# Optimization experiments

Hardware: AMD Instinct MI355X
Metric: run time of the kernel (lower is better)

The kernel has to match this reference:

```python
import jax, jax.numpy as jnp
import numpy as np

# ---- constants from the source module ----
NB = [[0,1,2,3],[0,1,4],[0,2,5],[0,3,6],[1,4,7],[2,5,8],[3,6,9],[4,7,10],[5,8,11],[6,9],[7,10],[8,11],[12,13,14,15],[12,13,16],[12,14,17],[12,15],[13,16,18],[14,17,19],[16,18,20],[17,19,21],[18,20,22],[19,21,23],[20,22],[21,23]]
PARENT = np.array([0,0,0,0,1,2,3,4,5,6,7,8,9,9,9,12,13,14,16,17,18,19,20,21])  # root parent sentinel handled separately
KJ, NV, PREG = 24, 6890, 200
LEN = np.array([len(n) for n in NB])
NBR_IDX = np.zeros((KJ,4), np.int32)
NBR_VALID = np.zeros((KJ,4), np.float32)
for k, n in enumerate(NB):
    NBR_IDX[k,:len(n)] = n; NBR_VALID[k,:len(n)] = 1.0
BETA_POS = np.zeros((KJ,17), np.float32); BETA_POS[np.arange(KJ), 4*LEN] = 1.0
SLICE_MASK = np.zeros((23,17), np.float32)
for j in range(23):
    SLICE_MASK[j,:4*LEN[j]+1] = 1.0  # self.K[j] has 4*len(NB[j])+1 rows
NBR_IDX = jnp.asarray(NBR_IDX); NBR_VALID = jnp.asarray(NBR_VALID)
BETA_POS = jnp.asarray(BETA_POS); SLICE_MASK = jnpp = jnp.asarray(SLICE_MASK)


def setup_inputs() -> dict:
    key = jax.random.key(0)
    ks = jax.random.split(key, 9)
    V = jax.random.normal(ks[0], (PREG, NV, 3), jnp.float32)
    T = jax.random.normal(ks[1], (PREG, NV, 3), jnp.float32)
    J = jax.random.normal(ks[2], (PREG, KJ, 3), jnp.float32)
    theta = 0.3 * jax.random.normal(ks[3], (PREG, 72), jnp.float32)
    W_prime = jax.random.uniform(ks[4], (NV, KJ), jnp.float32)
    W_i = jax.random.uniform(ks[5], (NV, KJ), jnp.float32)
    W_i = W_i / W_i.sum(axis=1, keepdims=True)
    A = jax.random.uniform(ks[6], (23, NV), jnp.float32)
    K_mats = 0.01 * jax.random.normal(ks[7], (23, 17, 3 * NV), jnp.float32)
    K_mats = K_mats * SLICE_MASK[:, :, None]  # zero rows beyond the ragged per-joint size
    beta_2 = jnp.ones((1,), jnp.float32)
    return {"V": V, "T": T, "J": J, "theta": theta, "W_prime": W_prime, "W_i": W_i, "A": A, "K_mats": K_mats, "beta_2": beta_2, "epoch": 1}


def _rodrigues(pose):  # pose: (K,3)
    angle = jnp.maximum(jnp.linalg.norm(pose, axis=1, keepdims=True), 1e-8)
    axis = pose / angle
    x, y, z = axis[:, 0], axis[:, 1], axis[:, 2]
    zero = jnp.zeros_like(x)
    skew = jnp.stack([zero, -z, y, z, zero, -x, -y, x, zero], axis=1).reshape(-1, 3, 3)
    outer = axis[:, :, None] * axis[:, None, :]
    c = jnp.cos(angle)[:, :, None]
    s = jnp.sin(angle)[:, :, None]
    eye = jnp.eye(3, dtype=pose.dtype)[None]
    return c * eye + (1.0 - c) * outer + s * skew


def _compute_G(pose72, Jp):  # pose72: (72,), Jp: (K,3) -> (K,4,4)
    R = _rodrigues(pose72.reshape(KJ, 3))
    t = Jp - jnp.concatenate([jnp.zeros((1, 3), Jp.dtype), Jp[PARENT[1:]]], axis=0)
    G_local = jnp.zeros((KJ, 4, 4), Jp.dtype)
    G_local = G_local.at[:, :3, :3].set(R).at[:, :3, 3].set(t).at[:, 3, 3].set(1.0)
    Gs = [G_local[0]]
    for i in range(1, KJ):  # fixed 24-joint kinematic tree
        Gs.append(Gs[PARENT[i]] @ G_local[i])
    G = jnp.stack(Gs, axis=0)
    off = jnp.einsum('kij,kj->ki', G[:, :3, :3], Jp)  # homogeneous w=0 -> rotation only
    return G.at[:, :3, 3].add(-off)


def _axis2quat(p):  # (M,3) -> (M,4)
    angle = jnp.sqrt(jnp.maximum(jnp.sum(p ** 2, axis=1), 1e-16))
    n = p / angle[:, None]
    s = jnp.sin(angle / 2)
    return jnp.stack([n[:, 0] * s, n[:, 1] * s, n[:, 2] * s, jnp.cos(angle / 2) - 1.0], axis=1)


def reference(V, T, J, theta, W_prime, W_i, A, K_mats, beta_2, epoch):
    P = V.shape[0]
    b2 = beta_2[0]
    # normalized skinning weights
    W_relu = jax.nn.relu(W_prime)
    W_change = W_relu / (W_relu.sum(axis=1, keepdims=True) + 1e-8)
    # per-pose global joint transforms
    G_prime = jax.vmap(_compute_G)(theta, J)  # (P,K,4,4)
    # quaternion features and blend-shape correction
    q = _axis2quat(theta.reshape(P * KJ, 3)).reshape(P, KJ, 4)
    qg = q[:, NBR_IDX, :] * NBR_VALID[None, :, :, None]       # (P,K,4,4) neighbor gather
    q17 = jnp.concatenate([qg.reshape(P, KJ, 16), jnp.zeros((P, KJ, 1), q.dtype)], axis=-1)
    q17 = q17 + BETA_POS[None] * b2                            # beta_2 at column 4*len
    qm = q17[:, 1:, :] * SLICE_MASK[None]                      # ragged slice q_ne[:, j+1, :lenK]
    contrib = jnp.einsum('pjl,jlm->pjm', qm, K_mats).reshape(P, 23, NV, 3)
    T_p = jnp.einsum('pjnc,jn->pnc', contrib, jax.nn.relu(A)) + T
    # linear blend skinning
    T_h = jnp.concatenate([T_p, jnp.ones((P, NV, 1), T_p.dtype)], axis=-1)
    transformed = jnp.einsum('pkij,pnj->pnki', G_prime[:, :, :3, :], T_h)  # (P,N,K,3)
    verts = jnp.einsum('nk,pnkc->pnc', W_change, transformed)
    # energies
    e = float(epoch)
    g_wi = 0.1 * np.exp(-0.1 * e)
    g_w = 0.002 * np.exp(-0.008 * e)
    g_a = 0.001 * np.exp(-0.008 * e)
    g_k = 0.1 * np.exp(-0.008 * e)
    E_D = jnp.sum((V - verts) ** 2)
    E_Wi = jnp.sum((W_change - W_i) ** 2)
    E_W = jnp.sum(jnp.abs(W_change))
    E_A = jnp.sum(jnp.abs(A))
    E_K = jnp.sum(jnp.sqrt(jnp.sum(K_mats ** 2, axis=(1, 2))))
    E = E_D + g_wi * E_Wi + g_w * E_W + g_a * E_A + g_k * E_K
    return (E, verts)
```

## Files before the change

kernel.cpp:

```cpp
#include <hip/hip_runtime.h>
#include <math.h>

#define KJ 24
#define NV 6890
#define PREG 200
#define M_TOT (NV*3)
#define KDIM 391
#define KPAD 416
#define TP_STRIDE 20672
#define NMTILE 323

#define EDP_OFF 0
#define EKP_OFF 2816
#define WIP_OFF 10248
#define EWP_OFF 10280
#define EAP_OFF 10312
#define RED_OFF 10344
#define G_OFF   10384
#define WT_OFF  67984
#define RA_OFF  233344
#define QBH_OFF_U 1417600
#define QBL_OFF_U 1524096
#define TP_OFF  815296

typedef __attribute__((ext_vector_type(8))) short short8;
typedef __attribute__((ext_vector_type(4))) float f32x4;

__constant__ int c_PARENT[24] = {0,0,0,0,1,2,3,4,5,6,7,8,9,9,9,12,13,14,16,17,18,19,20,21};
__constant__ int c_DEPTH[24]  = {0,1,1,1,2,2,2,3,3,3,4,4,4,4,4,5,5,5,6,6,7,7,8,8};
__constant__ int c_LEN[24]    = {4,3,3,3,3,3,3,3,3,2,2,2,4,3,3,2,3,3,3,3,3,3,2,2};
__constant__ int c_NBR[24][4] = {
  {0,1,2,3},{0,1,4,0},{0,2,5,0},{0,3,6,0},{1,4,7,0},{2,5,8,0},{3,6,9,0},{4,7,10,0},
  {5,8,11,0},{6,9,0,0},{7,10,0,0},{8,11,0,0},{12,13,14,15},{12,13,16,0},{12,14,17,0},
  {12,15,0,0},{13,16,18,0},{14,17,19,0},{16,18,20,0},{17,19,21,0},{18,20,22,0},
  {19,21,23,0},{20,22,0,0},{21,23,0,0}};

__device__ __forceinline__ float waveReduce(float v) {
  #pragma unroll
  for (int off = 32; off > 0; off >>= 1) v += __shfl_down(v, off, 64);
  return v;
}
__device__ __forceinline__ unsigned short f2bf(float x) {
  union { float f; unsigned u; } v; v.f = x;
  unsigned r = v.u + 0x7FFFu + ((v.u >> 16) & 1u);
  return (unsigned short)(r >> 16);
}
__device__ __forceinline__ float bf2f(unsigned short h) {
  union { unsigned u; float f; } v; v.u = ((unsigned)h) << 16; return v.f;
}

__global__ __launch_bounds__(256) void kPre(const float* __restrict__ J,
                                            const float* __restrict__ theta,
                                            const float* __restrict__ beta2,
                                            const float* __restrict__ Wp,
                                            const float* __restrict__ Wi,
                                            const float* __restrict__ A,
                                            float* __restrict__ ws) {
  unsigned short* qbh = (unsigned short*)ws + QBH_OFF_U;
  unsigned short* qbl = (unsigned short*)ws + QBL_OFF_U;
  int b = blockIdx.x;
  if (b < 50) {
    __shared__ float Gl[4][24][12];
    __shared__ float Gg[4][24][12];
    __shared__ float q[4][24][4];
    int w = threadIdx.x >> 6, t = threadIdx.x & 63;
    int p = b*4 + w;
    if (t < 24) {
      float x = theta[p*72 + 3*t + 0];
      float y = theta[p*72 + 3*t + 1];
      float z = theta[p*72 + 3*t + 2];
      float n2 = x*x + y*y + z*z;
      float ang = fmaxf(sqrtf(n2), 1e-8f);
      float ia = 1.f/ang;
      float ax = x*ia, ay = y*ia, az = z*ia;
      float c = cosf(ang), s = sinf(ang), C = 1.f - c;
      float jx = J[p*72+3*t], jy = J[p*72+3*t+1], jz = J[p*72+3*t+2];
      float tx = jx, ty = jy, tz = jz;
      if (t > 0) {
        int par = c_PARENT[t];
        tx -= J[p*72+3*par]; ty -= J[p*72+3*par+1]; tz -= J[p*72+3*par+2];
      }
      Gl[w][t][0]=c+C*ax*ax;   Gl[w][t][1]=C*ax*ay-s*az; Gl[w][t][2]=C*ax*az+s*ay; Gl[w][t][3]=tx;
      Gl[w][t][4]=C*ax*ay+s*az;Gl[w][t][5]=c+C*ay*ay;    Gl[w][t][6]=C*ay*az-s*ax; Gl[w][t][7]=ty;
      Gl[w][t][8]=C*ax*az-s*ay;Gl[w][t][9]=C*ay*az+s*ax; Gl[w][t][10]=c+C*az*az;   Gl[w][t][11]=tz;
      float ang2 = sqrtf(fmaxf(n2, 1e-16f));
      float inv2 = 1.f/ang2;
      float s2 = sinf(0.5f*ang2);
      q[w][t][0] = x*inv2*s2; q[w][t][1] = y*inv2*s2; q[w][t][2] = z*inv2*s2;
      q[w][t][3] = cosf(0.5f*ang2) - 1.f;
    }
    __syncthreads();
    for (int lev = 0; lev <= 8; lev++) {
      if (t < 24 && c_DEPTH[t] == lev) {
        if (lev == 0) {
          for (int i2 = 0; i2 < 12; i2++) Gg[w][0][i2] = Gl[w][0][i2];
        } else {
          int par = c_PARENT[t];
          for (int r = 0; r < 3; r++) {
            float g0 = Gg[w][par][r*4+0], g1 = Gg[w][par][r*4+1];
            float g2 = Gg[w][par][r*4+2], g3 = Gg[w][par][r*4+3];
            for (int c2 = 0; c2 < 4; c2++) {
              float v = g0*Gl[w][t][0+c2] + g1*Gl[w][t][4+c2] + g2*Gl[w][t][8+c2];
              if (c2 == 3) v += g3;
              Gg[w][t][r*4+c2] = v;
            }
          }
        }
      }
      __syncthreads();
    }
    if (t < 24) {
      float jx = J[p*72+3*t], jy = J[p*72+3*t+1], jz = J[p*72+3*t+2];
      float* gp = ws + G_OFF + p*288 + t*12;
      #pragma unroll
      for (int r = 0; r < 3; r++) {
        float off = Gg[w][t][r*4+0]*jx + Gg[w][t][r*4+1]*jy + Gg[w][t][r*4+2]*jz;
        Gg[w][t][r*4+3] -= off;
      }
      #pragma unroll
      for (int i2 = 0; i2 < 12; i2++) gp[i2] = Gg[w][t][i2];
    }
    __syncthreads();
    float b2 = beta2[0];
    for (int e = t; e < KDIM; e += 64) {
      int j = e / 17, l = e - 17*j;
      int k = j + 1;
      float val = 0.f;
      if (l < 4*c_LEN[j] + 1) {
        if (l < 16) {
          int sidx = l >> 2, cc = l & 3;
          if (sidx < c_LEN[k]) val = q[w][c_NBR[k][sidx]][cc];
        }
        if (l == 4*c_LEN[k]) val += b2;
      }
      unsigned short hi = f2bf(val);
      unsigned short lo = f2bf(val - bf2f(hi));
      qbh[p*KPAD + e] = hi;
      qbl[p*KPAD + e] = lo;
    }
    for (int e = KDIM + t; e < KPAD; e += 64) {
      qbh[p*KPAD + e] = 0; qbl[p*KPAD + e] = 0;
    }
  } else {
    int d = b - 50;
    int t = threadIdx.x;
    int n = d*256 + t;
    float ewi = 0.f, ew = 0.f, ea = 0.f;
    if (n < NV) {
      float wv[24]; float sum = 0.f;
      const float4* wp4 = (const float4*)(Wp + n*24);
      #pragma unroll
      for (int i = 0; i < 6; i++) {
        float4 v4 = wp4[i];
        wv[4*i+0] = fmaxf(v4.x, 0.f); wv[4*i+1] = fmaxf(v4.y, 0.f);
        wv[4*i+2] = fmaxf(v4.z, 0.f); wv[4*i+3] = fmaxf(v4.w, 0.f);
        sum += wv[4*i+0]+wv[4*i+1]+wv[4*i+2]+wv[4*i+3];
      }
      float inv = 1.f/(sum + 1e-8f);
      #pragma unroll
      for (int k = 0; k < 24; k++) {
        float wc = wv[k]*inv;
        ws[WT_OFF + k*NV + n] = wc;
        ew += fabsf(wc);
        float dd = wc - Wi[n*24+k];
        ewi += dd*dd;
      }
    }
    for (int i = d*256 + t; i < 23*NV; i += 27*256) ea += fabsf(A[i]);
    for (int i = d*256 + t; i < 23*TP_STRIDE; i += 27*256) {
      int j = i / TP_STRIDE, m = i - j*TP_STRIDE;
      float v = 0.f;
      if (m < M_TOT) v = fmaxf(A[j*NV + m/3], 0.f);
      ws[RA_OFF + i] = v;
    }
    for (int i = d*256 + t; i < 56*KPAD; i += 27*256) {
      qbh[200*KPAD + i] = 0; qbl[200*KPAD + i] = 0;
    }
    __shared__ float red[3][4];
    int lane = t & 63, wv2 = t >> 6;
    ewi = waveReduce(ewi); ew = waveReduce(ew); ea = waveReduce(ea);
    if (lane == 0) { red[0][wv2] = ewi; red[1][wv2] = ew; red[2][wv2] = ea; }
    __syncthreads();
    if (t == 0) {
      ws[WIP_OFF + d] = red[0][0]+red[0][1]+red[0][2]+red[0][3];
      ws[EWP_OFF + d] = red[1][0]+red[1][1]+red[1][2]+red[1][3];
      ws[EAP_OFF + d] = red[2][0]+red[2][1]+red[2][2]+red[2][3];
    }
  }
}

__global__ __launch_bounds__(256) void kB(const float* __restrict__ K,
                                          float* __restrict__ ws) {
  __shared__ unsigned short Bh[64*32];
  __shared__ unsigned short Bl[64*32];
  __shared__ float ek[23];
  const unsigned short* qbh = (const unsigned short*)ws + QBH_OFF_U;
  const unsigned short* qbl = (const unsigned short*)ws + QBL_OFF_U;
  float* __restrict__ TP = ws + TP_OFF;

  const int tid = threadIdx.x;
  const int bx = blockIdx.x;
  const int py = blockIdx.y;
  const int m0 = bx * 64;
  const int w = tid >> 6, lane = tid & 63;
  const int r = lane & 15, qd = lane >> 4;
  const int pbase = py*128 + w*32;
  const int c4 = tid & 15, pr = tid >> 4;

  if (tid < 23) ek[tid] = 0.f;
  __syncthreads();

  f32x4 acc[2][4];
  #pragma unroll
  for (int h = 0; h < 2; h++)
    #pragma unroll
    for (int f = 0; f < 4; f++) acc[h][f] = (f32x4){0.f,0.f,0.f,0.f};

  const int aoff0 = (pbase + r) * KPAD + qd * 8;
  const int aoff1 = aoff0 + 16 * KPAD;

  for (int ks = 0; ks < 13; ks++) {
    if (ks) __syncthreads();
    {
      int mm = m0 + 4*c4;
      int kg0 = ks*32 + 2*pr, kg1 = kg0 + 1;
      float ka[4] = {0,0,0,0}, kb[4] = {0,0,0,0};
      float wa[4] = {0,0,0,0}, wb[4] = {0,0,0,0};
      float sq0 = 0.f, sq1 = 0.f;
      if (kg0 < KDIM) {
        int j = kg0 / 17;
        const float* kr = K + (size_t)kg0*M_TOT + mm;
        if (mm + 3 < M_TOT) {
          float2 x = *(const float2*)kr; float2 y = *(const float2*)(kr+2);
          ka[0]=x.x; ka[1]=x.y; ka[2]=y.x; ka[3]=y.y;
        } else {
          #pragma unroll
          for (int i = 0; i < 4; i++) if (mm+i < M_TOT) ka[i] = kr[i];
        }
        const float* rr = ws + RA_OFF + (size_t)j*TP_STRIDE + mm;
        float4 ra = *(const float4*)rr;
        wa[0]=ka[0]*ra.x; wa[1]=ka[1]*ra.y; wa[2]=ka[2]*ra.z; wa[3]=ka[3]*ra.w;
        sq0 = ka[0]*ka[0]+ka[1]*ka[1]+ka[2]*ka[2]+ka[3]*ka[3];
      }
      if (kg1 < KDIM) {
        int j = kg1 / 17;
        const float* kr = K + (size_t)kg1*M_TOT + mm;
        if (mm + 3 < M_TOT) {
          float2 x = *(const float2*)kr; float2 y = *(const float2*)(kr+2);
          kb[0]=x.x; kb[1]=x.y; kb[2]=y.x; kb[3]=y.y;
        } else {
          #pragma unroll
          for (int i = 0; i < 4; i++) if (mm+i < M_TOT) kb[i] = kr[i];
        }
        const float* rr = ws + RA_OFF + (size_t)j*TP_STRIDE + mm;
        float4 ra = *(const float4*)rr;
        wb[0]=kb[0]*ra.x; wb[1]=kb[1]*ra.y; wb[2]=kb[2]*ra.z; wb[3]=kb[3]*ra.w;
        sq1 = kb[0]*kb[0]+kb[1]*kb[1]+kb[2]*kb[2]+kb[3]*kb[3];
      }
      #pragma unroll
      for (int i = 0; i < 4; i++) {
        unsigned short h0 = f2bf(wa[i]); unsigned short l0 = f2bf(wa[i] - bf2f(h0));
        unsigned short h1 = f2bf(wb[i]); unsigned short l1 = f2bf(wb[i] - bf2f(h1));
        int mi = 4*c4 + i;
        int physdw = (pr + 4*(c4 & 3)) & 15;
        *(unsigned*)&Bh[mi*32 + physdw*2] = (unsigned)h0 | ((unsigned)h1 << 16);
        *(unsigned*)&Bl[mi*32 + physdw*2] = (unsigned)l0 | ((unsigned)l1 << 16);
      }
      if (py == 0) {
        #pragma unroll
        for (int off = 1; off <= 8; off <<= 1) {
          sq0 += __shfl_xor(sq0, off, 64);
          sq1 += __shfl_xor(sq1, off, 64);
        }
        if ((lane & 15) == 0) {
          if (kg0 < KDIM) atomicAdd(&ek[kg0/17], sq0);
          if (kg1 < KDIM) atomicAdd(&ek[kg1/17], sq1);
        }
      }
    }
    __syncthreads();
    {
      int kso = ks * 32;
      short8 ah0 = *(const short8*)(qbh + aoff0 + kso);
      short8 ah1 = *(const short8*)(qbh + aoff1 + kso);
      short8 al0 = *(const short8*)(qbl + aoff0 + kso);
      short8 al1 = *(const short8*)(qbl + aoff1 + kso);
      short8 bh[4], bl[4];
      const int rotdw = 4*((r >> 2) & 3);
      #pragma unroll
      for (int f = 0; f < 4; f++) {
        int m = f*16 + r;
        int physdw = (4*qd + rotdw) & 15;
        bh[f] = *(const short8*)(&Bh[m*32 + physdw*2]);
        bl[f] = *(const short8*)(&Bl[m*32 + physdw*2]);
      }
      #pragma unroll
      for (int f = 0; f < 4; f++) {
        acc[0][f] = __builtin_amdgcn_mfma_f32_16x16x32_bf16(ah0, bh[f], acc[0][f], 0, 0, 0);
        acc[1][f] = __builtin_amdgcn_mfma_f32_16x16x32_bf16(ah1, bh[f], acc[1][f], 0, 0, 0);
      }
      #pragma unroll
      for (int f = 0; f < 4; f++) {
        acc[0][f] = __builtin_amdgcn_mfma_f32_16x16x32_bf16(ah0, bl[f], acc[0][f], 0, 0, 0);
        acc[1][f] = __builtin_amdgcn_mfma_f32_16x16x32_bf16(ah1, bl[f], acc[1][f], 0, 0, 0);
      }
      #pragma unroll
      for (int f = 0; f < 4; f++) {
        acc[0][f] = __builtin_amdgcn_mfma_f32_16x16x32_bf16(al0, bh[f], acc[0][f], 0, 0, 0);
        acc[1][f] = __builtin_amdgcn_mfma_f32_16x16x32_bf16(al1, bh[f], acc[1][f], 0, 0, 0);
      }
    }
  }
  #pragma unroll
  for (int h = 0; h < 2; h++)
    #pragma unroll
    for (int f = 0; f < 4; f++)
      #pragma unroll
      for (int g = 0; g < 4; g++) {
        int p = pbase + h*16 + qd*4 + g;
        TP[(size_t)p*TP_STRIDE + m0 + f*16 + r] = acc[h][f][g];
      }
  __syncthreads();
  if (py == 0 && tid < 23)
    ws[EKP_OFF + tid*NMTILE + bx] = ek[tid];
}

__global__ __launch_bounds__(256) void kC(const float* __restrict__ V,
                                          const float* __restrict__ T,
                                          float* __restrict__ ws,
                                          float* __restrict__ out) {
  int p = blockIdx.y;
  int n0 = (blockIdx.x*256 + threadIdx.x) * 2;
  __shared__ float Gs[288];
  __shared__ float tmp[4];
  if (threadIdx.x < 72)
    ((float4*)Gs)[threadIdx.x] = ((const float4*)(ws + G_OFF + p*288))[threadIdx.x];
  __syncthreads();
  float ed = 0.f;
  if (n0 < NV) {
    float M0[12], M1[12];
    #pragma unroll
    for (int i = 0; i < 12; i++) { M0[i] = 0.f; M1[i] = 0.f; }
    const float* Wt = ws + WT_OFF;
    #pragma unroll
    for (int k = 0; k < 24; k++) {
      float2 wv = *(const float2*)(Wt + k*NV + n0);
      float4 g0 = *(const float4*)(Gs + k*12 + 0);
      float4 g1 = *(const float4*)(Gs + k*12 + 4);
      float4 g2 = *(const float4*)(Gs + k*12 + 8);
      M0[0] = fmaf(wv.x, g0.x, M0[0]); M0[1]  = fmaf(wv.x, g0.y, M0[1]);
      M0[2] = fmaf(wv.x, g0.z, M0[2]); M0[3]  = fmaf(wv.x, g0.w, M0[3]);
      M0[4] = fmaf(wv.x, g1.x, M0[4]); M0[5]  = fmaf(wv.x, g1.y, M0[5]);
      M0[6] = fmaf(wv.x, g1.z, M0[6]); M0[7]  = fmaf(wv.x, g1.w, M0[7]);
      M0[8] = fmaf(wv.x, g2.x, M0[8]); M0[9]  = fmaf(wv.x, g2.y, M0[9]);
      M0[10]= fmaf(wv.x, g2.z, M0[10]);M0[11] = fmaf(wv.x, g2.w, M0[11]);
      M1[0] = fmaf(wv.y, g0.x, M1[0]); M1[1]  = fmaf(wv.y, g0.y, M1[1]);
      M1[2] = fmaf(wv.y, g0.z, M1[2]); M1[3]  = fmaf(wv.y, g0.w, M1[3]);
      M1[4] = fmaf(wv.y, g1.x, M1[4]); M1[5]  = fmaf(wv.y, g1.y, M1[5]);
      M1[6] = fmaf(wv.y, g1.z, M1[6]); M1[7]  = fmaf(wv.y, g1.w, M1[7]);
      M1[8] = fmaf(wv.y, g2.x, M1[8]); M1[9]  = fmaf(wv.y, g2.y, M1[9]);
      M1[10]= fmaf(wv.y, g2.z, M1[10]);M1[11] = fmaf(wv.y, g2.w, M1[11]);
    }
    size_t tb = (size_t)p*M_TOT + 3*n0;
    size_t pb = (size_t)p*TP_STRIDE + 3*n0;
    float2 q0 = *(const float2*)(ws + TP_OFF + pb);
    float2 q1 = *(const float2*)(ws + TP_OFF + pb + 2);
    float2 q2 = *(const float2*)(ws + TP_OFF + pb + 4);
    float2 s0 = *(const float2*)(T + tb);
    float2 s1 = *(const float2*)(T + tb + 2);
    float2 s2 = *(const float2*)(T + tb + 4);
    float ta0 = q0.x + s0.x, ta1 = q0.y + s0.y, ta2 = q1.x + s1.x;
    float tb0 = q1.y + s1.y, tb1 = q2.x + s2.x, tb2 = q2.y + s2.y;
    float v00 = M0[0]*ta0 + M0[1]*ta1 + M0[2]*ta2  + M0[3];
    float v01 = M0[4]*ta0 + M0[5]*ta1 + M0[6]*ta2  + M0[7];
    float v02 = M0[8]*ta0 + M0[9]*ta1 + M0[10]*ta2 + M0[11];
    float v10 = M1[0]*tb0 + M1[1]*tb1 + M1[2]*tb2  + M1[3];
    float v11 = M1[4]*tb0 + M1[5]*tb1 + M1[6]*tb2  + M1[7];
    float v12 = M1[8]*tb0 + M1[9]*tb1 + M1[10]*tb2 + M1[11];
    out[1+tb+0] = v00; out[1+tb+1] = v01; out[1+tb+2] = v02;
    out[1+tb+3] = v10; out[1+tb+4] = v11; out[1+tb+5] = v12;
    float2 x0 = *(const float2*)(V + tb);
    float2 x1 = *(const float2*)(V + tb + 2);
    float2 x2 = *(const float2*)(V + tb + 4);
    float d0 = x0.x-v00, d1 = x0.y-v01, d2 = x1.x-v02;
    float d3 = x1.y-v10, d4 = x2.x-v11, d5 = x2.y-v12;
    ed = d0*d0 + d1*d1 + d2*d2 + d3*d3 + d4*d4 + d5*d5;
  }
  ed = waveReduce(ed);
  int lane = threadIdx.x & 63, w = threadIdx.x >> 6;
  if (lane == 0) tmp[w] = ed;
  __syncthreads();
  if (threadIdx.x == 0)
    ws[EDP_OFF + blockIdx.y*14 + blockIdx.x] = tmp[0]+tmp[1]+tmp[2]+tmp[3];
}

__global__ __launch_bounds__(256) void kF1(float* __restrict__ ws) {
  __shared__ float sb[4];
  int b = blockIdx.x, t = threadIdx.x, lane = t & 63, w = t >> 6;
  if (b < 23) {
    float s = 0.f;
    for (int i = t; i < NMTILE; i += 256) s += ws[EKP_OFF + b*NMTILE + i];
    s = waveReduce(s);
    if (lane == 0) sb[w] = s;
    __syncthreads();
    if (t == 0) ws[RED_OFF + b] = sb[0]+sb[1]+sb[2]+sb[3];
  } else if (b == 23) {
    float s = 0.f;
    for (int i = t; i < 2800; i += 256) s += ws[EDP_OFF + i];
    s = waveReduce(s);
    if (lane == 0) sb[w] = s;
    __syncthreads();
    if (t == 0) ws[RED_OFF + 23] = sb[0]+sb[1]+sb[2]+sb[3];
  } else {
    if (w == 0) {
      float s = (lane < 27) ? ws[WIP_OFF + lane] : 0.f;
      s = waveReduce(s);
      if (lane == 0) ws[RED_OFF + 24] = s;
    } else if (w == 1) {
      float s = (lane < 27) ? ws[EWP_OFF + lane] : 0.f;
      s = waveReduce(s);
      if (lane == 0) ws[RED_OFF + 25] = s;
    } else if (w == 2) {
      float s = (lane < 27) ? ws[EAP_OFF + lane] : 0.f;
      s = waveReduce(s);
      if (lane == 0) ws[RED_OFF + 26] = s;
    }
  }
}

__global__ void kF2(const int* __restrict__ epoch, const float* __restrict__ ws,
                    float* __restrict__ out) {
  int t = threadIdx.x;
  float s = (t < 23) ? sqrtf(ws[RED_OFF + t]) : 0.f;
  s = waveReduce(s);
  if (t == 0) {
    float e    = (float)epoch[0];
    float g_wi = 0.1f   * expf(-0.1f  * e);
    float g_w  = 0.002f * expf(-0.008f* e);
    float g_a  = 0.001f * expf(-0.008f* e);
    float g_k  = 0.1f   * expf(-0.008f* e);
    out[0] = ws[RED_OFF+23] + g_wi*ws[RED_OFF+24] + g_w*ws[RED_OFF+25]
           + g_a*ws[RED_OFF+26] + g_k*s;
  }
}

extern "C" void kernel_launch(void* const* d_in, const int* in_sizes, int n_in,
                              void* d_out, int out_size, void* d_ws, size_t ws_size,
                              hipStream_t stream) {
  const float* V     = (const float*)d_in[0];
  const float* T     = (const float*)d_in[1];
  const float* J     = (const float*)d_in[2];
  const float* theta = (const float*)d_in[3];
  const float* Wp    = (const float*)d_in[4];
  const float* Wi    = (const float*)d_in[5];
  const float* A     = (const float*)d_in[6];
  const float* K     = (const float*)d_in[7];
  const float* b2    = (const float*)d_in[8];
  const int*   epoch = (const int*)d_in[9];
  float* out = (float*)d_out;
  float* ws  = (float*)d_ws;

  hipLaunchKernelGGL(kPre, dim3(77),         dim3(256), 0, stream,
                     J, theta, b2, Wp, Wi, A, ws);
  hipLaunchKernelGGL(kB,   dim3(NMTILE, 2),  dim3(256), 0, stream, K, ws);
  hipLaunchKernelGGL(kC,   dim3(14, PREG),   dim3(256), 0, stream, V, T, ws, out);
  hipLaunchKernelGGL(kF1,  dim3(25),         dim3(256), 0, stream, ws);
  hipLaunchKernelGGL(kF2,  dim3(1),          dim3(64),  0, stream, epoch, ws, out);
}
```

Before: 203.8 us.

## Process all 256 poses per K tile block and prefetch next K stage

Kernel kB no longer splits the pose dimension across two grid rows. Each block now computes all 256 (padded) pose rows for its 64-column K tile, so K and RA are read and converted to bf16 hi/lo only once instead of twice. The next K stage is loaded into registers while the current one is consumed (register double-buffering), and the LDS B tile uses a padded stride of 40 instead of a swizzle. The trade-off is a halved grid (323 blocks), more accumulator registers per thread (launch_bounds 256,2), and possibly lower occupancy and parallelism.

```diff
diff --git a/kernel.cpp b/kernel.cpp
--- a/kernel.cpp
+++ b/kernel.cpp
@@ -189,10 +189,10 @@
   }
 }
 
-__global__ __launch_bounds__(256) void kB(const float* __restrict__ K,
-                                          float* __restrict__ ws) {
-  __shared__ unsigned short Bh[64*32];
-  __shared__ unsigned short Bl[64*32];
+__global__ __launch_bounds__(256, 2) void kB(const float* __restrict__ K,
+                                             float* __restrict__ ws) {
+  __shared__ unsigned short Bh[64*40];
+  __shared__ unsigned short Bl[64*40];
   __shared__ float ek[23];
   const unsigned short* qbh = (const unsigned short*)ws + QBH_OFF_U;
   const unsigned short* qbl = (const unsigned short*)ws + QBL_OFF_U;
@@ -200,128 +200,118 @@
 
   const int tid = threadIdx.x;
   const int bx = blockIdx.x;
-  const int py = blockIdx.y;
   const int m0 = bx * 64;
   const int w = tid >> 6, lane = tid & 63;
   const int r = lane & 15, qd = lane >> 4;
-  const int pbase = py*128 + w*32;
   const int c4 = tid & 15, pr = tid >> 4;
 
   if (tid < 23) ek[tid] = 0.f;
-  __syncthreads();
-
-  f32x4 acc[2][4];
+
+  f32x4 acc[4][4];
   #pragma unroll
-  for (int h = 0; h < 2; h++)
+  for (int h = 0; h < 4; h++)
     #pragma unroll
     for (int f = 0; f < 4; f++) acc[h][f] = (f32x4){0.f,0.f,0.f,0.f};
 
-  const int aoff0 = (pbase + r) * KPAD + qd * 8;
-  const int aoff1 = aoff0 + 16 * KPAD;
-
+  int aoff[4];
+  #pragma unroll
+  for (int h = 0; h < 4; h++) aoff[h] = (w*64 + h*16 + r) * KPAD + qd * 8;
+
+  float wa[4], wb[4], sq0, sq1; int kg0, kg1;
+
+  auto load_stage = [&](int ks) {
+    int mm = m0 + 4*c4;
+    kg0 = ks*32 + 2*pr; kg1 = kg0 + 1;
+    float ka[4] = {0,0,0,0}, kc[4] = {0,0,0,0};
+    sq0 = 0.f; sq1 = 0.f;
+    #pragma unroll
+    for (int i = 0; i < 4; i++) { wa[i] = 0.f; wb[i] = 0.f; }
+    if (kg0 < KDIM) {
+      int j = kg0 / 17;
+      const float* kr = K + (size_t)kg0*M_TOT + mm;
+      if (mm + 3 < M_TOT) {
+        float2 x = *(const float2*)kr; float2 y = *(const float2*)(kr+2);
+        ka[0]=x.x; ka[1]=x.y; ka[2]=y.x; ka[3]=y.y;
+      } else {
+        #pragma unroll
+        for (int i = 0; i < 4; i++) if (mm+i < M_TOT) ka[i] = kr[i];
+      }
+      float4 ra = *(const float4*)(ws + RA_OFF + (size_t)j*TP_STRIDE + mm);
+      wa[0]=ka[0]*ra.x; wa[1]=ka[1]*ra.y; wa[2]=ka[2]*ra.z; wa[3]=ka[3]*ra.w;
+      sq0 = ka[0]*ka[0]+ka[1]*ka[1]+ka[2]*ka[2]+ka[3]*ka[3];
+    }
+    if (kg1 < KDIM) {
+      int j = kg1 / 17;
+      const float* kr = K + (size_t)kg1*M_TOT + mm;
+      if (mm + 3 < M_TOT) {
+        float2 x = *(const float2*)kr; float2 y = *(const float2*)(kr+2);
+        kc[0]=x.x; kc[1]=x.y; kc[2]=y.x; kc[3]=y.y;
+      } else {
+        #pragma unroll
+        for (int i = 0; i < 4; i++) if (mm+i < M_TOT) kc[i] = kr[i];
+      }
+      float4 ra = *(const float4*)(ws + RA_OFF + (size_t)j*TP_STRIDE + mm);
+      wb[0]=kc[0]*ra.x; wb[1]=kc[1]*ra.y; wb[2]=kc[2]*ra.z; wb[3]=kc[3]*ra.w;
+      sq1 = kc[0]*kc[0]+kc[1]*kc[1]+kc[2]*kc[2]+kc[3]*kc[3];
+    }
+  };
+  auto write_stage = [&]() {
+    #pragma unroll
+    for (int i = 0; i < 4; i++) {
+      unsigned short h0 = f2bf(wa[i]); unsigned short l0 = f2bf(wa[i] - bf2f(h0));
+      unsigned short h1 = f2bf(wb[i]); unsigned short l1 = f2bf(wb[i] - bf2f(h1));
+      int mi = 4*c4 + i;
+      *(unsigned*)&Bh[mi*40 + pr*2] = (unsigned)h0 | ((unsigned)h1 << 16);
+      *(unsigned*)&Bl[mi*40 + pr*2] = (unsigned)l0 | ((unsigned)l1 << 16);
+    }
+    #pragma unroll
+    for (int off = 1; off <= 8; off <<= 1) {
+      sq0 += __shfl_xor(sq0, off, 64);
+      sq1 += __shfl_xor(sq1, off, 64);
+    }
+    if ((lane & 15) == 0) {
+      if (kg0 < KDIM) atomicAdd(&ek[kg0/17], sq0);
+      if (kg1 < KDIM) atomicAdd(&ek[kg1/17], sq1);
+    }
+  };
+
+  load_stage(0);
   for (int ks = 0; ks < 13; ks++) {
-    if (ks) __syncthreads();
-    {
-      int mm = m0 + 4*c4;
-      int kg0 = ks*32 + 2*pr, kg1 = kg0 + 1;
-      float ka[4] = {0,0,0,0}, kb[4] = {0,0,0,0};
-      float wa[4] = {0,0,0,0}, wb[4] = {0,0,0,0};
-      float sq0 = 0.f, sq1 = 0.f;
-      if (kg0 < KDIM) {
-        int j = kg0 / 17;
-        const float* kr = K + (size_t)kg0*M_TOT + mm;
-        if (mm + 3 < M_TOT) {
-          float2 x = *(const float2*)kr; float2 y = *(const float2*)(kr+2);
-          ka[0]=x.x; ka[1]=x.y; ka[2]=y.x; ka[3]=y.y;
-        } else {
-          #pragma unroll
-          for (int i = 0; i < 4; i++) if (mm+i < M_TOT) ka[i] = kr[i];
-        }
-        const float* rr = ws + RA_OFF + (size_t)j*TP_STRIDE + mm;
-        float4 ra = *(const float4*)rr;
-        wa[0]=ka[0]*ra.x; wa[1]=ka[1]*ra.y; wa[2]=ka[2]*ra.z; wa[3]=ka[3]*ra.w;
-        sq0 = ka[0]*ka[0]+ka[1]*ka[1]+ka[2]*ka[2]+ka[3]*ka[3];
-      }
-      if (kg1 < KDIM) {
-        int j = kg1 / 17;
-        const float* kr = K + (size_t)kg1*M_TOT + mm;
-        if (mm + 3 < M_TOT) {
-          float2 x = *(const float2*)kr; float2 y = *(const float2*)(kr+2);
-          kb[0]=x.x; kb[1]=x.y; kb[2]=y.x; kb[3]=y.y;
-        } else {
-          #pragma unroll
-          for (int i = 0; i < 4; i++) if (mm+i < M_TOT) kb[i] = kr[i];
-        }
-        const float* rr = ws + RA_OFF + (size_t)j*TP_STRIDE + mm;
-        float4 ra = *(const float4*)rr;
-        wb[0]=kb[0]*ra.x; wb[1]=kb[1]*ra.y; wb[2]=kb[2]*ra.z; wb[3]=kb[3]*ra.w;
-        sq1 = kb[0]*kb[0]+kb[1]*kb[1]+kb[2]*kb[2]+kb[3]*kb[3];
-      }
-      #pragma unroll
-      for (int i = 0; i < 4; i++) {
-        unsigned short h0 = f2bf(wa[i]); unsigned short l0 = f2bf(wa[i] - bf2f(h0));
-        unsigned short h1 = f2bf(wb[i]); unsigned short l1 = f2bf(wb[i] - bf2f(h1));
-        int mi = 4*c4 + i;
-        int physdw = (pr + 4*(c4 & 3)) & 15;
-        *(unsigned*)&Bh[mi*32 + physdw*2] = (unsigned)h0 | ((unsigned)h1 << 16);
-        *(unsigned*)&Bl[mi*32 + physdw*2] = (unsigned)l0 | ((unsigned)l1 << 16);
-      }
-      if (py == 0) {
-        #pragma unroll
-        for (int off = 1; off <= 8; off <<= 1) {
-          sq0 += __shfl_xor(sq0, off, 64);
-          sq1 += __shfl_xor(sq1, off, 64);
-        }
-        if ((lane & 15) == 0) {
-          if (kg0 < KDIM) atomicAdd(&ek[kg0/17], sq0);
-          if (kg1 < KDIM) atomicAdd(&ek[kg1/17], sq1);
-        }
-      }
-    }
-    __syncthreads();
-    {
-      int kso = ks * 32;
-      short8 ah0 = *(const short8*)(qbh + aoff0 + kso);
-      short8 ah1 = *(const short8*)(qbh + aoff1 + kso);
-      short8 al0 = *(const short8*)(qbl + aoff0 + kso);
-      short8 al1 = *(const short8*)(qbl + aoff1 + kso);
-      short8 bh[4], bl[4];
-      const int rotdw = 4*((r >> 2) & 3);
-      #pragma unroll
-      for (int f = 0; f < 4; f++) {
-        int m = f*16 + r;
-        int physdw = (4*qd + rotdw) & 15;
-        bh[f] = *(const short8*)(&Bh[m*32 + physdw*2]);
-        bl[f] = *(const short8*)(&Bl[m*32 + physdw*2]);
-      }
-      #pragma unroll
-      for (int f = 0; f < 4; f++) {
-        acc[0][f] = __builtin_amdgcn_mfma_f32_16x16x32_bf16(ah0, bh[f], acc[0][f], 0, 0, 0);
-        acc[1][f] = __builtin_amdgcn_mfma_f32_16x16x32_bf16(ah1, bh[f], acc[1][f], 0, 0, 0);
-      }
-      #pragma unroll
-      for (int f = 0; f < 4; f++) {
-        acc[0][f] = __builtin_amdgcn_mfma_f32_16x16x32_bf16(ah0, bl[f], acc[0][f], 0, 0, 0);
-        acc[1][f] = __builtin_amdgcn_mfma_f32_16x16x32_bf16(ah1, bl[f], acc[1][f], 0, 0, 0);
-      }
-      #pragma unroll
-      for (int f = 0; f < 4; f++) {
-        acc[0][f] = __builtin_amdgcn_mfma_f32_16x16x32_bf16(al0, bh[f], acc[0][f], 0, 0, 0);
-        acc[1][f] = __builtin_amdgcn_mfma_f32_16x16x32_bf16(al1, bh[f], acc[1][f], 0, 0, 0);
+    __syncthreads();
+    write_stage();
+    if (ks + 1 < 13) load_stage(ks + 1);
+    __syncthreads();
+    int kso = ks * 32;
+    short8 ah[4], al[4];
+    #pragma unroll
+    for (int h = 0; h < 4; h++) {
+      ah[h] = *(const short8*)(qbh + aoff[h] + kso);
+      al[h] = *(const short8*)(qbl + aoff[h] + kso);
+    }
+    #pragma unroll
+    for (int f = 0; f < 4; f++) {
+      int m = f*16 + r;
+      short8 bh = *(const short8*)(&Bh[m*40 + qd*8]);
+      short8 bl = *(const short8*)(&Bl[m*40 + qd*8]);
+      #pragma unroll
+      for (int h = 0; h < 4; h++) {
+        acc[h][f] = __builtin_amdgcn_mfma_f32_16x16x32_bf16(ah[h], bh, acc[h][f], 0, 0, 0);
+        acc[h][f] = __builtin_amdgcn_mfma_f32_16x16x32_bf16(ah[h], bl, acc[h][f], 0, 0, 0);
+        acc[h][f] = __builtin_amdgcn_mfma_f32_16x16x32_bf16(al[h], bh, acc[h][f], 0, 0, 0);
       }
     }
   }
   #pragma unroll
-  for (int h = 0; h < 2; h++)
+  for (int h = 0; h < 4; h++)
     #pragma unroll
     for (int f = 0; f < 4; f++)
       #pragma unroll
       for (int g = 0; g < 4; g++) {
-        int p = pbase + h*16 + qd*4 + g;
+        int p = w*64 + h*16 + qd*4 + g;
         TP[(size_t)p*TP_STRIDE + m0 + f*16 + r] = acc[h][f][g];
       }
   __syncthreads();
-  if (py == 0 && tid < 23)
+  if (tid < 23)
     ws[EKP_OFF + tid*NMTILE + bx] = ek[tid];
 }
 
@@ -460,10 +450,10 @@
   float* out = (float*)d_out;
   float* ws  = (float*)d_ws;
 
-  hipLaunchKernelGGL(kPre, dim3(77),         dim3(256), 0, stream,
+  hipLaunchKernelGGL(kPre, dim3(77),       dim3(256), 0, stream,
                      J, theta, b2, Wp, Wi, A, ws);
-  hipLaunchKernelGGL(kB,   dim3(NMTILE, 2),  dim3(256), 0, stream, K, ws);
-  hipLaunchKernelGGL(kC,   dim3(14, PREG),   dim3(256), 0, stream, V, T, ws, out);
-  hipLaunchKernelGGL(kF1,  dim3(25),         dim3(256), 0, stream, ws);
-  hipLaunchKernelGGL(kF2,  dim3(1),          dim3(64),  0, stream, epoch, ws, out);
-}
+  hipLaunchKernelGGL(kB,   dim3(NMTILE),   dim3(256), 0, stream, K, ws);
+  hipLaunchKernelGGL(kC,   dim3(14, PREG), dim3(256), 0, stream, V, T, ws, out);
+  hipLaunchKernelGGL(kF1,  dim3(25),       dim3(256), 0, stream, ws);
+  hipLaunchKernelGGL(kF2,  dim3(1),        dim3(64),  0, stream, epoch, ws, out);
+}
```

New measurement: 207.4 us. About the same (+1.8%).
